# Kernel tuning notes

Hardware: AMD Instinct MI355X
Metric: run time of the kernel (lower is better)

The kernel has to match this reference:

```python
import jax, jax.numpy as jnp
import numpy as np

H = 8   # num_heads
K = 7   # kernel_size


def setup_inputs() -> dict:
    key = jax.random.key(0)
    k1, k2, k3 = jax.random.split(key, 3)
    T, B, C = 2048, 16, 512
    x = jax.random.normal(k1, (T, B, C), dtype=jnp.float32)
    query = jax.random.normal(k2, (T, B, C), dtype=jnp.float32)
    W = jax.random.normal(k3, (C, H * K), dtype=jnp.float32) * 0.02
    return {"x": x, "query": query, "W": W}


def reference(x, query, W):
    T, B, C = x.shape
    R = C // H
    # per-position, per-head kernel weights: Dense(H*K) on query, no bias
    weight = jnp.einsum('tbc,cn->tbn', query, W).reshape(T * B * H, K)
    weight = jax.nn.softmax(weight, axis=-1)  # weight_softmax=True; dropout rate 0 is identity
    # TF extract_patches with SAME padding along T: total pad K-1, more on the bottom
    pad_before = (K - 1) // 2
    pad_after = K - 1 - pad_before
    x_pad = jnp.pad(x, ((pad_before, pad_after), (0, 0), (0, 0)))
    idx = jnp.arange(T)[:, None] + jnp.arange(K)[None, :]  # (T, K)
    patches = x_pad[idx]                      # (T, K, B, C)
    patches = jnp.transpose(patches, (0, 2, 1, 3))  # (T, B, K, C): TF depth order is (k, c)
    # Faithful to the source: flat (K*C) axis reinterpreted as (H, R, K)
    x_unfold = patches.reshape(T * B * H, R, K)
    out = jnp.einsum('nrk,nk->nr', x_unfold, weight)  # batched tiny matmul
    return out.reshape(T, B, C)
```

## Files before the change

### kernel.cpp

```cpp
#include <hip/hip_runtime.h>

#define T_DIM 2048
#define B_DIM 16
#define C_DIM 512
#define NW 56
#define XS_BYTES (22 * 512 * 2)
#define A_OFF    XS_BYTES
#define WT_OFF   (XS_BYTES + 4160)
#define LDS_TOTAL (XS_BYTES + 16384)

typedef __attribute__((ext_vector_type(8))) short short8;
typedef __attribute__((ext_vector_type(4))) float floatx4;

static __device__ __forceinline__ unsigned short f2bf(float x) {
    union { float f; unsigned u; } v; v.f = x;
    return (unsigned short)((v.u + 0x7FFFu + ((v.u >> 16) & 1u)) >> 16);
}
static __device__ __forceinline__ float bf_lo(unsigned u) {
    union { unsigned u; float f; } c; c.u = u << 16; return c.f;
}
static __device__ __forceinline__ float bf_hi(unsigned u) {
    union { unsigned u; float f; } c; c.u = u & 0xFFFF0000u; return c.f;
}
static __device__ __forceinline__ int swz(int a) { return a ^ ((a >> 3) & 0x70); }

__global__ __launch_bounds__(256)
void pack_w(const float* __restrict__ W, short8* __restrict__ Bg) {
    const int g  = blockIdx.x * 256 + threadIdx.x;
    const int ks = g >> 8;
    const int nt = (g >> 6) & 3;
    const int l  = g & 63;
    const int n  = nt * 16 + (l & 15);
    const int k0 = ks * 32 + ((l >> 4) & 3) * 8;
    short8 o;
#pragma unroll
    for (int j = 0; j < 8; ++j) {
        const float v = (n < NW) ? W[(size_t)(k0 + j) * NW + n] : 0.f;
        o[j] = (short)f2bf(v);
    }
    Bg[g] = o;
}

__global__ __launch_bounds__(256)
void fused_kernel(const float* __restrict__ x, const float* __restrict__ q,
                  const short8* __restrict__ Bg, float* __restrict__ out) {
    __shared__ __align__(16) char S[LDS_TOTAL];

    const int tid  = threadIdx.x;
    const int lane = tid & 63;
    const int wv   = tid >> 6;
    const int b    = blockIdx.x & 15;
    const int t0   = (blockIdx.x >> 4) * 16;

    const int rq = lane & 15;
    const int qq = lane >> 4;
    const float* qrow = q + ((size_t)(t0 + rq) * B_DIM + b) * C_DIM + qq * 8;
    float4 qr[4][2];
#pragma unroll
    for (int s = 0; s < 4; ++s) {
        const int ks = wv + s * 4;
        qr[s][0] = *(const float4*)(qrow + ks * 32);
        qr[s][1] = *(const float4*)(qrow + ks * 32 + 4);
    }
    short8 bfr[16];
#pragma unroll
    for (int ks = 0; ks < 16; ++ks)
        bfr[ks] = Bg[(ks * 4 + wv) * 64 + lane];
    float4 xr[11];
#pragma unroll
    for (int j = 0; j < 11; ++j) {
        const int idx = tid + j * 256;
        const int i   = idx >> 7;
        const int c   = (idx & 127) * 4;
        const int tp  = t0 + i - 3;
        xr[j] = make_float4(0.f, 0.f, 0.f, 0.f);
        if (tp >= 0 && tp < T_DIM)
            xr[j] = *(const float4*)(x + ((size_t)tp * B_DIM + b) * C_DIM + c);
    }

    short8* A8 = (short8*)(S + A_OFF);
#pragma unroll
    for (int s = 0; s < 4; ++s) {
        const int ks = wv + s * 4;
        short8 o;
        o[0] = (short)f2bf(qr[s][0].x); o[1] = (short)f2bf(qr[s][0].y);
        o[2] = (short)f2bf(qr[s][0].z); o[3] = (short)f2bf(qr[s][0].w);
        o[4] = (short)f2bf(qr[s][1].x); o[5] = (short)f2bf(qr[s][1].y);
        o[6] = (short)f2bf(qr[s][1].z); o[7] = (short)f2bf(qr[s][1].w);
        A8[ks * 64 + lane] = o;
    }
    __syncthreads();

    floatx4 acc = (floatx4){0.f, 0.f, 0.f, 0.f};
#pragma unroll
    for (int ks = 0; ks < 16; ++ks) {
        const short8 af = A8[ks * 64 + lane];
        acc = __builtin_amdgcn_mfma_f32_16x16x32_bf16(af, bfr[ks], acc, 0, 0, 0);
    }

    char* XS = S;
#pragma unroll
    for (int j = 0; j < 11; ++j) {
        const int idx = tid + j * 256;
        uint2 p;
        p.x = (unsigned)f2bf(xr[j].x) | ((unsigned)f2bf(xr[j].y) << 16);
        p.y = (unsigned)f2bf(xr[j].z) | ((unsigned)f2bf(xr[j].w) << 16);
        const int a = idx * 8;
        *(uint2*)(XS + swz(a)) = p;
    }
    __syncthreads();

    float* L = (float*)(S + A_OFF);
    const int m = lane & 15;
    const int quad = lane >> 4;
#pragma unroll
    for (int r = 0; r < 4; ++r)
        L[(quad * 4 + r) * 65 + wv * 16 + m] = acc[r];
    __syncthreads();

    float* wt = (float*)(S + WT_OFF);
    if (tid < 128) {
        const int row = tid >> 3, h = tid & 7;
        const float* Lp = L + row * 65 + h * 7;
        float mx = Lp[0];
#pragma unroll
        for (int k = 1; k < 7; ++k) mx = fmaxf(mx, Lp[k]);
        float e[7], sm = 0.f;
#pragma unroll
        for (int k = 0; k < 7; ++k) { e[k] = __expf(Lp[k] - mx); sm += e[k]; }
        const float inv = 1.0f / sm;
#pragma unroll
        for (int k = 0; k < 7; ++k) wt[row * NW + h * 7 + k] = e[k] * inv;
    }
    __syncthreads();

    const int h = lane >> 3;
    const int base_b = lane * 112;
#pragma unroll
    for (int s = 0; s < 4; ++s) {
        const int tt = wv * 4 + s;
        const int tb = tt * 1024 + base_b;
        uint4 xu[7];
#pragma unroll
        for (int i = 0; i < 7; ++i)
            xu[i] = *(const uint4*)(XS + swz(tb + i * 16));
        float xf[56];
#pragma unroll
        for (int i = 0; i < 7; ++i) {
            xf[i * 8 + 0] = bf_lo(xu[i].x); xf[i * 8 + 1] = bf_hi(xu[i].x);
            xf[i * 8 + 2] = bf_lo(xu[i].y); xf[i * 8 + 3] = bf_hi(xu[i].y);
            xf[i * 8 + 4] = bf_lo(xu[i].z); xf[i * 8 + 5] = bf_hi(xu[i].z);
            xf[i * 8 + 6] = bf_lo(xu[i].w); xf[i * 8 + 7] = bf_hi(xu[i].w);
        }
        const float* wp = wt + tt * NW + h * 7;
        float w[7];
#pragma unroll
        for (int k = 0; k < 7; ++k) w[k] = wp[k];
        float a8[8];
#pragma unroll
        for (int r = 0; r < 8; ++r) {
            float sacc = xf[r * 7] * w[0];
#pragma unroll
            for (int k = 1; k < 7; ++k) sacc = fmaf(w[k], xf[r * 7 + k], sacc);
            a8[r] = sacc;
        }
        float* orow = out + ((size_t)(t0 + tt) * B_DIM + b) * C_DIM + lane * 8;
        *(float4*)(orow)     = make_float4(a8[0], a8[1], a8[2], a8[3]);
        *(float4*)(orow + 4) = make_float4(a8[4], a8[5], a8[6], a8[7]);
    }
}

extern "C" void kernel_launch(void* const* d_in, const int* in_sizes, int n_in,
                              void* d_out, int out_size, void* d_ws, size_t ws_size,
                              hipStream_t stream) {
    const float* x = (const float*)d_in[0];
    const float* q = (const float*)d_in[1];
    const float* W = (const float*)d_in[2];
    float* out = (float*)d_out;
    short8* Bg = (short8*)d_ws;

    pack_w<<<16, 256, 0, stream>>>(W, Bg);
    fused_kernel<<<(T_DIM / 16) * B_DIM, 256, 0, stream>>>(x, q, Bg, out);
}
```

Before: 174.5 us.

## Read x directly from global in fp32 instead of staging bf16 tile in LDS

Drops the LDS staging of the x window, which was converted to bf16 and swizzled. Each thread now loads its 56 fp32 x values straight from global memory, relying on cache for the overlapping windows. The launch bounds are raised to request 4 blocks per CU, and the LDS footprint shrinks. Precision of x improves, but global and cache traffic rises because each x row is re-read by several output rows, and the global load latency is no longer hidden behind the MFMA stage.

```diff
diff --git a/kernel.cpp b/kernel.cpp
--- a/kernel.cpp
+++ b/kernel.cpp
@@ -4,10 +4,6 @@
 #define B_DIM 16
 #define C_DIM 512
 #define NW 56
-#define XS_BYTES (22 * 512 * 2)
-#define A_OFF    XS_BYTES
-#define WT_OFF   (XS_BYTES + 4160)
-#define LDS_TOTAL (XS_BYTES + 16384)
 
 typedef __attribute__((ext_vector_type(8))) short short8;
 typedef __attribute__((ext_vector_type(4))) float floatx4;
@@ -16,13 +12,6 @@
     union { float f; unsigned u; } v; v.f = x;
     return (unsigned short)((v.u + 0x7FFFu + ((v.u >> 16) & 1u)) >> 16);
 }
-static __device__ __forceinline__ float bf_lo(unsigned u) {
-    union { unsigned u; float f; } c; c.u = u << 16; return c.f;
-}
-static __device__ __forceinline__ float bf_hi(unsigned u) {
-    union { unsigned u; float f; } c; c.u = u & 0xFFFF0000u; return c.f;
-}
-static __device__ __forceinline__ int swz(int a) { return a ^ ((a >> 3) & 0x70); }
 
 __global__ __launch_bounds__(256)
 void pack_w(const float* __restrict__ W, short8* __restrict__ Bg) {
@@ -41,10 +30,12 @@
     Bg[g] = o;
 }
 
-__global__ __launch_bounds__(256)
+__global__ __launch_bounds__(256, 4)
 void fused_kernel(const float* __restrict__ x, const float* __restrict__ q,
                   const short8* __restrict__ Bg, float* __restrict__ out) {
-    __shared__ __align__(16) char S[LDS_TOTAL];
+    __shared__ __align__(16) short8 A8[16 * 64];
+    __shared__ float L[16 * 65];
+    __shared__ float wt[16 * NW];
 
     const int tid  = threadIdx.x;
     const int lane = tid & 63;
@@ -52,76 +43,43 @@
     const int b    = blockIdx.x & 15;
     const int t0   = (blockIdx.x >> 4) * 16;
 
-    const int rq = lane & 15;
-    const int qq = lane >> 4;
-    const float* qrow = q + ((size_t)(t0 + rq) * B_DIM + b) * C_DIM + qq * 8;
-    float4 qr[4][2];
-#pragma unroll
-    for (int s = 0; s < 4; ++s) {
-        const int ks = wv + s * 4;
-        qr[s][0] = *(const float4*)(qrow + ks * 32);
-        qr[s][1] = *(const float4*)(qrow + ks * 32 + 4);
-    }
     short8 bfr[16];
 #pragma unroll
     for (int ks = 0; ks < 16; ++ks)
         bfr[ks] = Bg[(ks * 4 + wv) * 64 + lane];
-    float4 xr[11];
-#pragma unroll
-    for (int j = 0; j < 11; ++j) {
-        const int idx = tid + j * 256;
-        const int i   = idx >> 7;
-        const int c   = (idx & 127) * 4;
-        const int tp  = t0 + i - 3;
-        xr[j] = make_float4(0.f, 0.f, 0.f, 0.f);
-        if (tp >= 0 && tp < T_DIM)
-            xr[j] = *(const float4*)(x + ((size_t)tp * B_DIM + b) * C_DIM + c);
-    }
 
-    short8* A8 = (short8*)(S + A_OFF);
+    const int rq = lane & 15;
+    const int qq = lane >> 4;
+    const float* qrow = q + ((size_t)(t0 + rq) * B_DIM + b) * C_DIM + qq * 8;
 #pragma unroll
     for (int s = 0; s < 4; ++s) {
         const int ks = wv + s * 4;
+        const float4 v0 = *(const float4*)(qrow + ks * 32);
+        const float4 v1 = *(const float4*)(qrow + ks * 32 + 4);
         short8 o;
-        o[0] = (short)f2bf(qr[s][0].x); o[1] = (short)f2bf(qr[s][0].y);
-        o[2] = (short)f2bf(qr[s][0].z); o[3] = (short)f2bf(qr[s][0].w);
-        o[4] = (short)f2bf(qr[s][1].x); o[5] = (short)f2bf(qr[s][1].y);
-        o[6] = (short)f2bf(qr[s][1].z); o[7] = (short)f2bf(qr[s][1].w);
+        o[0] = (short)f2bf(v0.x); o[1] = (short)f2bf(v0.y);
+        o[2] = (short)f2bf(v0.z); o[3] = (short)f2bf(v0.w);
+        o[4] = (short)f2bf(v1.x); o[5] = (short)f2bf(v1.y);
+        o[6] = (short)f2bf(v1.z); o[7] = (short)f2bf(v1.w);
         A8[ks * 64 + lane] = o;
     }
     __syncthreads();
 
     floatx4 acc = (floatx4){0.f, 0.f, 0.f, 0.f};
 #pragma unroll
-    for (int ks = 0; ks < 16; ++ks) {
-        const short8 af = A8[ks * 64 + lane];
-        acc = __builtin_amdgcn_mfma_f32_16x16x32_bf16(af, bfr[ks], acc, 0, 0, 0);
-    }
+    for (int ks = 0; ks < 16; ++ks)
+        acc = __builtin_amdgcn_mfma_f32_16x16x32_bf16(A8[ks * 64 + lane], bfr[ks],
+                                                      acc, 0, 0, 0);
 
-    char* XS = S;
-#pragma unroll
-    for (int j = 0; j < 11; ++j) {
-        const int idx = tid + j * 256;
-        uint2 p;
-        p.x = (unsigned)f2bf(xr[j].x) | ((unsigned)f2bf(xr[j].y) << 16);
-        p.y = (unsigned)f2bf(xr[j].z) | ((unsigned)f2bf(xr[j].w) << 16);
-        const int a = idx * 8;
-        *(uint2*)(XS + swz(a)) = p;
-    }
-    __syncthreads();
-
-    float* L = (float*)(S + A_OFF);
-    const int m = lane & 15;
-    const int quad = lane >> 4;
+    const int m = lane & 15, quad = lane >> 4;
 #pragma unroll
     for (int r = 0; r < 4; ++r)
         L[(quad * 4 + r) * 65 + wv * 16 + m] = acc[r];
     __syncthreads();
 
-    float* wt = (float*)(S + WT_OFF);
     if (tid < 128) {
         const int row = tid >> 3, h = tid & 7;
-        const float* Lp = L + row * 65 + h * 7;
+        const float* Lp = &L[row * 65 + h * 7];
         float mx = Lp[0];
 #pragma unroll
         for (int k = 1; k < 7; ++k) mx = fmaxf(mx, Lp[k]);
@@ -134,25 +92,25 @@
     }
     __syncthreads();
 
-    const int h = lane >> 3;
-    const int base_b = lane * 112;
+    const int f0 = lane * 56;
+    const int hh = lane >> 3;
 #pragma unroll
     for (int s = 0; s < 4; ++s) {
         const int tt = wv * 4 + s;
-        const int tb = tt * 1024 + base_b;
-        uint4 xu[7];
-#pragma unroll
-        for (int i = 0; i < 7; ++i)
-            xu[i] = *(const uint4*)(XS + swz(tb + i * 16));
+        const int tb = t0 + tt - 3;
         float xf[56];
 #pragma unroll
-        for (int i = 0; i < 7; ++i) {
-            xf[i * 8 + 0] = bf_lo(xu[i].x); xf[i * 8 + 1] = bf_hi(xu[i].x);
-            xf[i * 8 + 2] = bf_lo(xu[i].y); xf[i * 8 + 3] = bf_hi(xu[i].y);
-            xf[i * 8 + 4] = bf_lo(xu[i].z); xf[i * 8 + 5] = bf_hi(xu[i].z);
-            xf[i * 8 + 6] = bf_lo(xu[i].w); xf[i * 8 + 7] = bf_hi(xu[i].w);
+        for (int i = 0; i < 14; ++i) {
+            const int f = f0 + i * 4;
+            const int d = f >> 9;
+            const int c = f & 511;
+            const int tp = tb + d;
+            float4 v = make_float4(0.f, 0.f, 0.f, 0.f);
+            if ((unsigned)tp < (unsigned)T_DIM)
+                v = *(const float4*)(x + ((size_t)tp * B_DIM + b) * C_DIM + c);
+            *(float4*)(&xf[i * 4]) = v;
         }
-        const float* wp = wt + tt * NW + h * 7;
+        const float* wp = &wt[tt * NW + hh * 7];
         float w[7];
 #pragma unroll
         for (int k = 0; k < 7; ++k) w[k] = wp[k];
```

Result: slower. 248.1 us (+42.1%).
